# Kernel tuning notes

Hardware: AMD Instinct MI355X
Metric: run time of the kernel (lower is better)

The kernel has to match this reference:

```python
import jax, jax.numpy as jnp
import numpy as np

# Memristor nonideality constants (from disturbed_outputs_i_v_non_linear)
G_MIN = 1e-4
G_MAX = 5e-4
K_V = 1.05
V_REF = jnp.array([-1.2, -0.9, -0.6, -0.3, 0.0, 0.3, 0.6, 0.9, 1.2], dtype=jnp.float32)
G_REF = jnp.array([0.0, 1e-4, 3e-4, 5e-4], dtype=jnp.float32)
I_REF = jnp.array([
    [0, 0, 0, 0, 0, 0, 0, 0, 0],
    [-1.5e-4, -1.1e-4, -7e-5, -3e-5, 0, 3e-5, 7e-5, 1.1e-4, 1.5e-4],
    [-5e-4, -3.5e-4, -2.2e-4, -9e-5, 0, 9e-5, 2.2e-4, 3.5e-4, 5e-4],
    [-9e-4, -6e-4, -3.7e-4, -1.5e-4, 0, 1.5e-4, 3.7e-4, 6e-4, 9e-4],
], dtype=jnp.float32)


def setup_inputs() -> dict:
    key = jax.random.key(0)
    k1, k2, k3 = jax.random.split(key, 3)
    n_in, n_out, batch = 1024, 1024, 128
    stdv = 1.0 / np.sqrt(n_in)
    x = jax.random.uniform(k1, (batch, n_in), dtype=jnp.float32)  # pixel-like inputs in [0,1]
    w = jax.random.normal(k2, (n_in, n_out), dtype=jnp.float32) * stdv  # RandomNormal(stddev=1/sqrt(n_in))
    b = jax.random.normal(k3, (n_out,), dtype=jnp.float32) * 0.01
    return {"x": x, "w": w, "b": b}


def reference(x, w, b):
    """Faithful jax port of memristor_dense.call: augment input with ones column,
    stack bias under weights, then nonlinear memristor I-V crossbar product."""
    B = x.shape[0]
    weights = jnp.concatenate([w, b[None, :]], axis=0)              # [N1, M], N1 = n_in+1
    inputs = jnp.concatenate([x, jnp.ones((B, 1), x.dtype)], axis=1)  # [B, N1]
    N1, M = weights.shape

    # w -> effective conductance (differential-pair effective mapping)
    max_weight = jnp.max(jnp.abs(weights))
    k_G = (G_MAX - G_MIN) / max_weight
    G_eff = k_G * weights                                            # [N1, M], signed
    V = K_V * inputs                                                 # [B, N1]

    # 1) interpolate reference I-V curve along V for each conductance level
    #    (jnp.interp clamps outside the V_REF grid, matching lookup-table behavior)
    I_at_V = jax.vmap(lambda Ir: jnp.interp(V, V_REF, Ir))(I_REF)    # [L, B, N1]

    # 2) linear interpolation along G on |G_eff| (odd symmetry in G via sign)
    Gabs = jnp.abs(G_eff)                                            # [N1, M]
    L = G_REF.shape[0]
    idx = jnp.clip(jnp.searchsorted(G_REF, Gabs, side='right') - 1, 0, L - 2)  # [N1, M]
    g0 = G_REF[idx]
    g1 = G_REF[idx + 1]
    t = ((Gabs - g0) / (g1 - g0))[:, :, None]                        # [N1, M, 1]

    jidx = jnp.arange(N1)[:, None]                                   # [N1, 1] broadcasts with idx
    I_lo = I_at_V[idx, :, jidx]                                      # [N1, M, B]
    I_hi = I_at_V[idx + 1, :, jidx]                                  # [N1, M, B]
    sgn = jnp.sign(G_eff)[:, :, None]
    I_ind = sgn * ((1.0 - t) * I_lo + t * I_hi)                      # per-device currents [N1, M, B]

    I_total = jnp.sum(I_ind, axis=0).T                               # [B, M]

    # current -> output: y = I / (k_V * k_G); reduces to x @ W for an ideal linear device
    y = I_total / (K_V * k_G)
    return y
```

## Files before the change

### kernel.cpp

```cpp
#include <hip/hip_runtime.h>
#include <hip/hip_bf16.h>
#include <cstdint>

#define K_V_C   1.05f
#define G_DIFF  4.0e-4f
#define KP4     4608

typedef __attribute__((ext_vector_type(8))) short short8;
typedef __attribute__((ext_vector_type(4))) float f32x4;

__device__ __constant__ float c_I1[9] = {-0.00015f,-0.00011f,-7e-05f,-3e-05f,0.f,3e-05f,7e-05f,0.00011f,0.00015f};
__device__ __constant__ float c_I2[9] = {-0.0005f,-0.00035f,-0.00022f,-9e-05f,0.f,9e-05f,0.00022f,0.00035f,0.0005f};
__device__ __constant__ float c_I3[9] = {-0.0009f,-0.0006f,-0.00037f,-0.00015f,0.f,0.00015f,0.00037f,0.0006f,0.0009f};

__device__ inline unsigned short f2bf(float f) {
  unsigned int u = __float_as_uint(f);
  u += 0x7FFFu + ((u >> 16) & 1u);
  return (unsigned short)(u >> 16);
}

__device__ inline float bf2f(unsigned short h) {
  return __uint_as_float((unsigned int)h << 16);
}

__device__ inline void interp3(float v, float& u1, float& u2, float& u3) {
  const float sf = v * 3.3333333333333335f + 4.0f;
  float fs = floorf(sf);
  fs = fminf(fmaxf(fs, 0.f), 7.f);
  const int   s  = (int)fs;
  const float fr = fminf(fmaxf(sf - fs, 0.f), 1.f);
  u1 = fmaf(fr, c_I1[s+1] - c_I1[s], c_I1[s]);
  u2 = fmaf(fr, c_I2[s+1] - c_I2[s], c_I2[s]);
  u3 = fmaf(fr, c_I3[s+1] - c_I3[s], c_I3[s]);
}

__device__ inline void coeff3f(float g, float& c1, float& c2, float& c3) {
  const float    ga = fabsf(g);
  const unsigned sb = __float_as_uint(g) & 0x80000000u;
  const float t1 = fminf(ga * 1e4f, 1.f);
  const float t2 = fminf(fmaxf((ga - 1e-4f) * 5e3f, 0.f), 1.f);
  const float t3 = fmaxf((ga - 3e-4f) * 5e3f, 0.f);
  c1 = __uint_as_float(__float_as_uint(t1 - t2) | sb);
  c2 = __uint_as_float(__float_as_uint(t2 - t3) | sb);
  c3 = __uint_as_float(__float_as_uint(t3) | sb);
}

__device__ inline void coeff3(float g, float& c1, float& c2, float& c3) {
  const float ga  = fabsf(g);
  const float sgn = (g > 0.f) ? 1.f : ((g < 0.f) ? -1.f : 0.f);
  const int   idx = (ga >= 3e-4f) ? 2 : ((ga >= 1e-4f) ? 1 : 0);
  const float g0   = (idx == 0) ? 0.f : ((idx == 1) ? 1e-4f : 3e-4f);
  const float invd = (idx == 0) ? 1e4f : 5e3f;
  const float t    = (ga - g0) * invd;
  const float clo = sgn * (1.f - t), chi = sgn * t;
  c1 = (idx == 0) ? chi : ((idx == 1) ? clo : 0.f);
  c2 = (idx == 1) ? chi : ((idx == 2) ? clo : 0.f);
  c3 = (idx == 2) ? chi : 0.f;
}

__global__ __launch_bounds__(256) void prep1_kernel(
    const float* __restrict__ x, const float* __restrict__ w,
    const float* __restrict__ bias, float* __restrict__ partials,
    unsigned short* __restrict__ Ub) {
  const int t = threadIdx.x, bid = blockIdx.x;
  if (bid < 1024) {
    const int i = bid * 256 + t;
    const float4 v = ((const float4*)w)[i];
    float m = fmaxf(fmaxf(fabsf(v.x), fabsf(v.y)), fmaxf(fabsf(v.z), fabsf(v.w)));
    if (i < 256) {
      const float4 bv = ((const float4*)bias)[i];
      m = fmaxf(m, fmaxf(fmaxf(fabsf(bv.x), fabsf(bv.y)),
                         fmaxf(fabsf(bv.z), fabsf(bv.w))));
    }
    #pragma unroll
    for (int o = 32; o > 0; o >>= 1) m = fmaxf(m, __shfl_down(m, o, 64));
    __shared__ float red[4];
    if ((t & 63) == 0) red[t >> 6] = m;
    __syncthreads();
    if (t == 0)
      partials[bid] = fmaxf(fmaxf(red[0], red[1]), fmaxf(red[2], red[3]));
  } else {
    const int idx = (bid - 1024) * 256 + t;
    const int b = idx / 288, j4 = idx - b * 288;
    ushort4 o0 = make_ushort4(0,0,0,0), o1 = o0, o2 = o0, o3 = o0;
    if (j4 < 256) {
      const float4 xv = ((const float4*)x)[b * 256 + j4];
      float u1, u2, u3;
      interp3(K_V_C * xv.x, u1, u2, u3); o0 = make_ushort4(f2bf(u1), f2bf(u2), f2bf(u3), 0);
      interp3(K_V_C * xv.y, u1, u2, u3); o1 = make_ushort4(f2bf(u1), f2bf(u2), f2bf(u3), 0);
      interp3(K_V_C * xv.z, u1, u2, u3); o2 = make_ushort4(f2bf(u1), f2bf(u2), f2bf(u3), 0);
      interp3(K_V_C * xv.w, u1, u2, u3); o3 = make_ushort4(f2bf(u1), f2bf(u2), f2bf(u3), 0);
    } else if (j4 == 256) {
      float u1, u2, u3;
      interp3(K_V_C, u1, u2, u3);
      o0 = make_ushort4(f2bf(u1), f2bf(u2), f2bf(u3), 0);
    }
    ushort4* dst = (ushort4*)(Ub + (size_t)b * KP4 + j4 * 16);
    dst[0] = o0; dst[1] = o1; dst[2] = o2; dst[3] = o3;
  }
}

__global__ __launch_bounds__(1024, 4) void fusedgemm_kernel(
    const float* __restrict__ w, const float* __restrict__ bias,
    const float* __restrict__ partials, const unsigned short* __restrict__ Ub,
    float* __restrict__ out) {
  __shared__ __align__(16) unsigned short panel[36864];
  const int t = threadIdx.x;
  const int wv = t >> 6, lane = t & 63, la = lane & 15, kg = lane >> 4;
  const int b0 = (blockIdx.x >> 5) * 16;
  const int n0 = (blockIdx.x & 31) * 32;

  #pragma unroll
  for (int i = 0; i < 8; ++i) {
    const int idx = i * 1024 + t;
    const int row = idx >> 3, c4 = idx & 7;
    const float4 v = *(const float4*)(w + (size_t)row * 1024 + n0 + c4 * 4);
    *(ushort4*)&panel[row * 32 + c4 * 4] =
        make_ushort4(f2bf(v.x), f2bf(v.y), f2bf(v.z), f2bf(v.w));
  }
  if (t < 32) panel[1024 * 32 + t] = f2bf(bias[n0 + t]);
  for (int i = 1025 * 32 + t; i < 1152 * 32; i += 1024) panel[i] = 0;

  float mx = 0.f;
  #pragma unroll
  for (int i = 0; i < 4; ++i) {
    const float4 p = ((const float4*)partials)[lane + i * 64];
    mx = fmaxf(mx, fmaxf(fmaxf(p.x, p.y), fmaxf(p.z, p.w)));
  }
  #pragma unroll
  for (int o = 1; o < 64; o <<= 1) mx = fmaxf(mx, __shfl_xor(mx, o, 64));
  const float maxw = mx;
  const float kG   = G_DIFF / maxw;
  __syncthreads();

  const unsigned short* Ap = Ub + (size_t)(b0 + la) * KP4 + wv * 288 + kg * 8;
  const int jb = wv * 72 + kg * 2;
  f32x4 acc0 = {0.f, 0.f, 0.f, 0.f};
  f32x4 acc1 = {0.f, 0.f, 0.f, 0.f};
  #pragma unroll 3
  for (int ks = 0; ks < 9; ++ks) {
    const short8 a = *(const short8*)(Ap + ks * 32);
    const int j0 = jb + ks * 8;
    const float w0a = bf2f(panel[j0 * 32 + la]);
    const float w0b = bf2f(panel[(j0 + 1) * 32 + la]);
    const float w1a = bf2f(panel[j0 * 32 + 16 + la]);
    const float w1b = bf2f(panel[(j0 + 1) * 32 + 16 + la]);
    float a1, a2, a3, b1, b2, b3, c1, c2, c3, d1, d2, d3;
    coeff3f(kG * w0a, a1, a2, a3);
    coeff3f(kG * w0b, b1, b2, b3);
    coeff3f(kG * w1a, c1, c2, c3);
    coeff3f(kG * w1b, d1, d2, d3);
    union { __hip_bfloat162 h[4]; short8 s; } bf0, bf1;
    bf0.h[0] = __float22bfloat162_rn(make_float2(a1, a2));
    bf0.h[1] = __float22bfloat162_rn(make_float2(a3, 0.f));
    bf0.h[2] = __float22bfloat162_rn(make_float2(b1, b2));
    bf0.h[3] = __float22bfloat162_rn(make_float2(b3, 0.f));
    bf1.h[0] = __float22bfloat162_rn(make_float2(c1, c2));
    bf1.h[1] = __float22bfloat162_rn(make_float2(c3, 0.f));
    bf1.h[2] = __float22bfloat162_rn(make_float2(d1, d2));
    bf1.h[3] = __float22bfloat162_rn(make_float2(d3, 0.f));
    acc0 = __builtin_amdgcn_mfma_f32_16x16x32_bf16(a, bf0.s, acc0, 0, 0, 0);
    acc1 = __builtin_amdgcn_mfma_f32_16x16x32_bf16(a, bf1.s, acc1, 0, 0, 0);
  }

  float* P = (float*)panel;
  __syncthreads();
  *(float4*)&P[wv * 512 + lane * 4]       = make_float4(acc0[0], acc0[1], acc0[2], acc0[3]);
  *(float4*)&P[wv * 512 + 256 + lane * 4] = make_float4(acc1[0], acc1[1], acc1[2], acc1[3]);
  __syncthreads();
  if (t < 512) {
    float s = 0.f;
    #pragma unroll
    for (int ww = 0; ww < 16; ++ww) s += P[ww * 512 + t];
    const int frag = t >> 8, f = t & 255;
    const int l2 = f >> 2, ai = f & 3;
    const int row = b0 + ((l2 >> 4) << 2) + ai;
    const int col = n0 + frag * 16 + (l2 & 15);
    out[(size_t)row * 1024 + col] = s * (maxw * (1.0f / (K_V_C * G_DIFF)));
  }
}

__global__ __launch_bounds__(256) void maxabs_atomic_kernel(
    const float* __restrict__ w, const float* __restrict__ b,
    unsigned int* __restrict__ wsmax) {
  const int NW4 = 262144, NB4 = 256;
  float m = 0.f;
  for (int i = blockIdx.x * blockDim.x + threadIdx.x; i < NW4 + NB4;
       i += gridDim.x * blockDim.x) {
    float4 v = (i < NW4) ? ((const float4*)w)[i] : ((const float4*)b)[i - NW4];
    m = fmaxf(m, fmaxf(fmaxf(fabsf(v.x), fabsf(v.y)),
                       fmaxf(fabsf(v.z), fabsf(v.w))));
  }
  #pragma unroll
  for (int o = 32; o > 0; o >>= 1) m = fmaxf(m, __shfl_down(m, o, 64));
  __shared__ float red[4];
  if ((threadIdx.x & 63) == 0) red[threadIdx.x >> 6] = m;
  __syncthreads();
  if (threadIdx.x == 0)
    atomicMax(wsmax, __float_as_uint(fmaxf(fmaxf(red[0], red[1]),
                                           fmaxf(red[2], red[3]))));
}

__global__ __launch_bounds__(256) void memristor_atomic_kernel(
    const float* __restrict__ x, const float* __restrict__ w,
    const float* __restrict__ bias, const unsigned int* __restrict__ wsmax,
    float* __restrict__ out) {
  __shared__ float4 U[2048];
  const int tid = threadIdx.x;
  const float maxw  = __uint_as_float(*wsmax);
  const float kG    = G_DIFF / maxw;
  const float scale = maxw * (1.0f / (K_V_C * G_DIFF));
  const int mq = tid & 15, bg = tid >> 4;
  const int m0 = blockIdx.x * 64 + mq * 4;
  const int swz = bg & 7;
  float acc[4][8];
  #pragma unroll
  for (int a = 0; a < 4; ++a)
    #pragma unroll
    for (int c = 0; c < 8; ++c) acc[a][c] = 0.f;
  for (int sc = blockIdx.y; sc < 65; sc += 16) {
    const int j0 = sc * 16;
    const int nj = min(16, 1025 - j0);
    __syncthreads();
    #pragma unroll
    for (int k = 0; k < 8; ++k) {
      const int e = k * 256 + tid;
      const int jl = e & 15, b = e >> 4;
      const int jg = j0 + jl;
      if (jg <= 1024) {
        const float v = (jg < 1024) ? K_V_C * x[b * 1024 + jg] : K_V_C;
        float u1, u2, u3;
        interp3(v, u1, u2, u3);
        U[b * 16 + (jl ^ ((b >> 3) & 7))] = make_float4(0.f, u1, u2, u3);
      }
    }
    __syncthreads();
    for (int jl = 0; jl < nj; ++jl) {
      const int jg = j0 + jl;
      const float4 wv = (jg < 1024) ? *(const float4*)(w + jg * 1024 + m0)
                                    : *(const float4*)(bias + m0);
      const float warr[4] = {wv.x, wv.y, wv.z, wv.w};
      float c1[4], c2[4], c3[4];
      #pragma unroll
      for (int mi = 0; mi < 4; ++mi) coeff3(kG * warr[mi], c1[mi], c2[mi], c3[mi]);
      const int base = bg * 128 + (jl ^ swz);
      #pragma unroll
      for (int bb = 0; bb < 8; ++bb) {
        const float4 u = U[base + bb * 16];
        #pragma unroll
        for (int mi = 0; mi < 4; ++mi)
          acc[mi][bb] = fmaf(c1[mi], u.y, fmaf(c2[mi], u.z, fmaf(c3[mi], u.w, acc[mi][bb])));
      }
    }
  }
  #pragma unroll
  for (int bb = 0; bb < 8; ++bb) {
    const int b = bg * 8 + bb;
    #pragma unroll
    for (int mi = 0; mi < 4; ++mi)
      atomicAdd(&out[b * 1024 + m0 + mi], acc[mi][bb] * scale);
  }
}

extern "C" void kernel_launch(void* const* d_in, const int* in_sizes, int n_in,
                              void* d_out, int out_size, void* d_ws, size_t ws_size,
                              hipStream_t stream) {
  const float* x = (const float*)d_in[0];
  const float* w = (const float*)d_in[1];
  const float* b = (const float*)d_in[2];
  float* out = (float*)d_out;

  float*          partials = (float*)((char*)d_ws + 128);
  unsigned short* Ub = (unsigned short*)((char*)d_ws + 8192);
  const size_t need = 8192 + (size_t)128 * KP4 * 2;

  if (ws_size >= need) {
    prep1_kernel<<<1168, 256, 0, stream>>>(x, w, b, partials, Ub);
    fusedgemm_kernel<<<256, 1024, 0, stream>>>(w, b, partials, Ub, out);
  } else {
    unsigned int* wsmax = (unsigned int*)d_ws;
    hipMemsetAsync(wsmax, 0, 4, stream);
    maxabs_atomic_kernel<<<256, 256, 0, stream>>>(w, b, wsmax);
    hipMemsetAsync(out, 0, (size_t)out_size * sizeof(float), stream);
    dim3 grid(16, 16);
    memristor_atomic_kernel<<<grid, 256, 0, stream>>>(x, w, b, wsmax, out);
  }
}
```

Before: 18.30 us.

## Fuse input I-V interpolation into GEMM kernel, dropping precomputed bf16 activation buffer

```diff
diff --git a/kernel.cpp b/kernel.cpp
--- a/kernel.cpp
+++ b/kernel.cpp
@@ -4,7 +4,6 @@
 
 #define K_V_C   1.05f
 #define G_DIFF  4.0e-4f
-#define KP4     4608
 
 typedef __attribute__((ext_vector_type(8))) short short8;
 typedef __attribute__((ext_vector_type(4))) float f32x4;
@@ -58,57 +57,43 @@
   c3 = (idx == 2) ? chi : 0.f;
 }
 
-__global__ __launch_bounds__(256) void prep1_kernel(
+__global__ __launch_bounds__(256) void maxabs_kernel(
+    const float* __restrict__ w, const float* __restrict__ bias,
+    float* __restrict__ partials) {
+  const int t = threadIdx.x, bid = blockIdx.x;
+  const int i = bid * 256 + t;
+  const float4 v = ((const float4*)w)[i];
+  float m = fmaxf(fmaxf(fabsf(v.x), fabsf(v.y)), fmaxf(fabsf(v.z), fabsf(v.w)));
+  if (i < 256) {
+    const float4 bv = ((const float4*)bias)[i];
+    m = fmaxf(m, fmaxf(fmaxf(fabsf(bv.x), fabsf(bv.y)),
+                       fmaxf(fabsf(bv.z), fabsf(bv.w))));
+  }
+  #pragma unroll
+  for (int o = 32; o > 0; o >>= 1) m = fmaxf(m, __shfl_down(m, o, 64));
+  __shared__ float red[4];
+  if ((t & 63) == 0) red[t >> 6] = m;
+  __syncthreads();
+  if (t == 0)
+    partials[bid] = fmaxf(fmaxf(red[0], red[1]), fmaxf(red[2], red[3]));
+}
+
+__global__ __launch_bounds__(1024, 4) void fusedgemm_kernel(
     const float* __restrict__ x, const float* __restrict__ w,
-    const float* __restrict__ bias, float* __restrict__ partials,
-    unsigned short* __restrict__ Ub) {
-  const int t = threadIdx.x, bid = blockIdx.x;
-  if (bid < 1024) {
-    const int i = bid * 256 + t;
-    const float4 v = ((const float4*)w)[i];
-    float m = fmaxf(fmaxf(fabsf(v.x), fabsf(v.y)), fmaxf(fabsf(v.z), fabsf(v.w)));
-    if (i < 256) {
-      const float4 bv = ((const float4*)bias)[i];
-      m = fmaxf(m, fmaxf(fmaxf(fabsf(bv.x), fabsf(bv.y)),
-                         fmaxf(fabsf(bv.z), fabsf(bv.w))));
-    }
-    #pragma unroll
-    for (int o = 32; o > 0; o >>= 1) m = fmaxf(m, __shfl_down(m, o, 64));
-    __shared__ float red[4];
-    if ((t & 63) == 0) red[t >> 6] = m;
-    __syncthreads();
-    if (t == 0)
-      partials[bid] = fmaxf(fmaxf(red[0], red[1]), fmaxf(red[2], red[3]));
-  } else {
-    const int idx = (bid - 1024) * 256 + t;
-    const int b = idx / 288, j4 = idx - b * 288;
-    ushort4 o0 = make_ushort4(0,0,0,0), o1 = o0, o2 = o0, o3 = o0;
-    if (j4 < 256) {
-      const float4 xv = ((const float4*)x)[b * 256 + j4];
-      float u1, u2, u3;
-      interp3(K_V_C * xv.x, u1, u2, u3); o0 = make_ushort4(f2bf(u1), f2bf(u2), f2bf(u3), 0);
-      interp3(K_V_C * xv.y, u1, u2, u3); o1 = make_ushort4(f2bf(u1), f2bf(u2), f2bf(u3), 0);
-      interp3(K_V_C * xv.z, u1, u2, u3); o2 = make_ushort4(f2bf(u1), f2bf(u2), f2bf(u3), 0);
-      interp3(K_V_C * xv.w, u1, u2, u3); o3 = make_ushort4(f2bf(u1), f2bf(u2), f2bf(u3), 0);
-    } else if (j4 == 256) {
-      float u1, u2, u3;
-      interp3(K_V_C, u1, u2, u3);
-      o0 = make_ushort4(f2bf(u1), f2bf(u2), f2bf(u3), 0);
-    }
-    ushort4* dst = (ushort4*)(Ub + (size_t)b * KP4 + j4 * 16);
-    dst[0] = o0; dst[1] = o1; dst[2] = o2; dst[3] = o3;
-  }
-}
-
-__global__ __launch_bounds__(1024, 4) void fusedgemm_kernel(
-    const float* __restrict__ w, const float* __restrict__ bias,
-    const float* __restrict__ partials, const unsigned short* __restrict__ Ub,
+    const float* __restrict__ bias, const float* __restrict__ partials,
     float* __restrict__ out) {
   __shared__ __align__(16) unsigned short panel[36864];
+  __shared__ __align__(16) float4 T0s[8], TDs[8];
   const int t = threadIdx.x;
   const int wv = t >> 6, lane = t & 63, la = lane & 15, kg = lane >> 4;
   const int b0 = (blockIdx.x >> 5) * 16;
   const int n0 = (blockIdx.x & 31) * 32;
+
+  if (t < 8) {
+    T0s[t] = make_float4(c_I1[t], c_I2[t], c_I3[t], 0.f);
+    TDs[t] = make_float4(c_I1[t+1] - c_I1[t], c_I2[t+1] - c_I2[t],
+                         c_I3[t+1] - c_I3[t], 0.f);
+  }
 
   #pragma unroll
   for (int i = 0; i < 8; ++i) {
@@ -133,14 +118,39 @@
   const float kG   = G_DIFF / maxw;
   __syncthreads();
 
-  const unsigned short* Ap = Ub + (size_t)(b0 + la) * KP4 + wv * 288 + kg * 8;
+  const float* xrow = x + (size_t)(b0 + la) * 1024;
   const int jb = wv * 72 + kg * 2;
   f32x4 acc0 = {0.f, 0.f, 0.f, 0.f};
   f32x4 acc1 = {0.f, 0.f, 0.f, 0.f};
   #pragma unroll 3
   for (int ks = 0; ks < 9; ++ks) {
-    const short8 a = *(const short8*)(Ap + ks * 32);
     const int j0 = jb + ks * 8;
+    const float xa = (j0     < 1024) ? xrow[min(j0, 1023)]     : 1.0f;
+    const float xb = (j0 + 1 < 1024) ? xrow[min(j0 + 1, 1023)] : 1.0f;
+    float u1, u2, u3, v1, v2, v3;
+    {
+      const float sf = (K_V_C * xa) * 3.3333333333333335f + 4.0f;
+      float fs = fminf(fmaxf(floorf(sf), 0.f), 7.f);
+      const int s = (int)fs;
+      const float fr = fminf(fmaxf(sf - fs, 0.f), 1.f);
+      const float4 y0 = T0s[s], dy = TDs[s];
+      u1 = fmaf(fr, dy.x, y0.x); u2 = fmaf(fr, dy.y, y0.y); u3 = fmaf(fr, dy.z, y0.z);
+    }
+    {
+      const float sf = (K_V_C * xb) * 3.3333333333333335f + 4.0f;
+      float fs = fminf(fmaxf(floorf(sf), 0.f), 7.f);
+      const int s = (int)fs;
+      const float fr = fminf(fmaxf(sf - fs, 0.f), 1.f);
+      const float4 y0 = T0s[s], dy = TDs[s];
+      v1 = fmaf(fr, dy.x, y0.x); v2 = fmaf(fr, dy.y, y0.y); v3 = fmaf(fr, dy.z, y0.z);
+    }
+    if (j0 > 1024)     { u1 = 0.f; u2 = 0.f; u3 = 0.f; }
+    if (j0 + 1 > 1024) { v1 = 0.f; v2 = 0.f; v3 = 0.f; }
+    union { __hip_bfloat162 h[4]; short8 s; } af;
+    af.h[0] = __float22bfloat162_rn(make_float2(u1, u2));
+    af.h[1] = __float22bfloat162_rn(make_float2(u3, 0.f));
+    af.h[2] = __float22bfloat162_rn(make_float2(v1, v2));
+    af.h[3] = __float22bfloat162_rn(make_float2(v3, 0.f));
     const float w0a = bf2f(panel[j0 * 32 + la]);
     const float w0b = bf2f(panel[(j0 + 1) * 32 + la]);
     const float w1a = bf2f(panel[j0 * 32 + 16 + la]);
@@ -159,8 +169,8 @@
     bf1.h[1] = __float22bfloat162_rn(make_float2(c3, 0.f));
     bf1.h[2] = __float22bfloat162_rn(make_float2(d1, d2));
     bf1.h[3] = __float22bfloat162_rn(make_float2(d3, 0.f));
-    acc0 = __builtin_amdgcn_mfma_f32_16x16x32_bf16(a, bf0.s, acc0, 0, 0, 0);
-    acc1 = __builtin_amdgcn_mfma_f32_16x16x32_bf16(a, bf1.s, acc1, 0, 0, 0);
+    acc0 = __builtin_amdgcn_mfma_f32_16x16x32_bf16(af.s, bf0.s, acc0, 0, 0, 0);
+    acc1 = __builtin_amdgcn_mfma_f32_16x16x32_bf16(af.s, bf1.s, acc1, 0, 0, 0);
   }
 
   float* P = (float*)panel;
@@ -270,13 +280,12 @@
   const float* b = (const float*)d_in[2];
   float* out = (float*)d_out;
 
-  float*          partials = (float*)((char*)d_ws + 128);
-  unsigned short* Ub = (unsigned short*)((char*)d_ws + 8192);
-  const size_t need = 8192 + (size_t)128 * KP4 * 2;
+  float* partials = (float*)((char*)d_ws + 128);
+  const size_t need = 128 + 1024 * sizeof(float);
 
   if (ws_size >= need) {
-    prep1_kernel<<<1168, 256, 0, stream>>>(x, w, b, partials, Ub);
-    fusedgemm_kernel<<<256, 1024, 0, stream>>>(w, b, partials, Ub, out);
+    maxabs_kernel<<<1024, 256, 0, stream>>>(w, b, partials);
+    fusedgemm_kernel<<<256, 1024, 0, stream>>>(x, w, b, partials, out);
   } else {
     unsigned int* wsmax = (unsigned int*)d_ws;
     hipMemsetAsync(wsmax, 0, 4, stream);
```

New measurement: 22.36 us. +22.2%, slower.
